# Optimization experiments

Measured on AMD Instinct MI355X. Metric: run time of the kernel, lower is better.

Reference implementation:

```python
import jax, jax.numpy as jnp
import numpy as np

B, N, C, H = 8, 1024, 1024, 16
HD = C // H
SCALE = HD ** -0.5

def setup_inputs() -> dict:
    key = jax.random.key(0)
    k1, k2, k3, k4 = jax.random.split(key, 4)
    x = jax.random.normal(k1, (B, N, C), dtype=jnp.float32)
    # torch nn.Linear weights: [out, in]
    w_qkv = jax.random.normal(k2, (3 * C, C), dtype=jnp.float32) * (C ** -0.5)
    w_proj = jax.random.normal(k3, (C, C), dtype=jnp.float32) * (C ** -0.5)
    b_proj = jax.random.normal(k4, (C,), dtype=jnp.float32) * 0.02
    return {"x": x, "w_qkv": w_qkv, "w_proj": w_proj, "b_proj": b_proj}

def reference(x, w_qkv, w_proj, b_proj):
    Bv, Nv, Cv = x.shape
    # qkv projection (no bias); torch Linear: x @ W^T
    qkv = jnp.einsum('bnc,dc->bnd', x, w_qkv)
    qkv = qkv.reshape(Bv, Nv, 3, H, HD).transpose(2, 0, 3, 1, 4)  # [3,B,H,N,hd]
    q, k, v = qkv[0], qkv[1], qkv[2]
    attn = jnp.einsum('bhnd,bhmd->bhnm', q, k) * SCALE  # [B,H,N,N]
    attn = jax.nn.softmax(attn, axis=-1)
    out = jnp.einsum('bhnm,bhmd->bhnd', attn, v)
    out = out.transpose(0, 2, 1, 3).reshape(Bv, Nv, Cv)
    out = jnp.einsum('bnc,dc->bnd', out, w_proj) + b_proj
    return out
```

## Files before the change

kernel.cpp:

```cpp
#include <hip/hip_runtime.h>


typedef __attribute__((ext_vector_type(8))) short bf16x8;
typedef __attribute__((ext_vector_type(4))) short bf16x4;
typedef __attribute__((ext_vector_type(4))) float f32x4;

__device__ __forceinline__ short f2bf(float f) {
    union { float f; unsigned u; } x;
    x.f = f;
    unsigned r = x.u + 0x7fffu + ((x.u >> 16) & 1u);
    return (short)(r >> 16);
}

__device__ __forceinline__ void load_lds16(const void* g, void* l) {
    __builtin_amdgcn_global_load_lds((const __attribute__((address_space(1))) unsigned*)g,
                                     (__attribute__((address_space(3))) unsigned*)l,
                                     16, 0, 0);
}

__global__ __launch_bounds__(256) void convert_all(const float* __restrict__ x,
                                                   const float* __restrict__ wqkv,
                                                   const float* __restrict__ wproj,
                                                   short* __restrict__ xb,
                                                   short* __restrict__ wqkvb,
                                                   short* __restrict__ wprojb) {
    int i = blockIdx.x * 256 + threadIdx.x;
    const float* src;
    short* dst;
    int j;
    if (i < 2097152)      { src = x;     dst = xb;     j = i; }
    else if (i < 2883584) { src = wqkv;  dst = wqkvb;  j = i - 2097152; }
    else                  { src = wproj; dst = wprojb; j = i - 2883584; }
    float4 v = *(const float4*)(src + j * 4);
    unsigned lo = (unsigned short)f2bf(v.x) | ((unsigned)(unsigned short)f2bf(v.y) << 16);
    unsigned hi = (unsigned short)f2bf(v.z) | ((unsigned)(unsigned short)f2bf(v.w) << 16);
    uint2 p; p.x = lo; p.y = hi;
    *(uint2*)(dst + j * 4) = p;
}

__global__ __launch_bounds__(256) void gemm_qkv(const short* __restrict__ A,
                                                const short* __restrict__ Bt,
                                                short* __restrict__ q,
                                                short* __restrict__ k,
                                                short* __restrict__ vt) {
    __shared__ alignas(16) short As[3][128][32];
    __shared__ alignas(16) short Bs[3][128][32];
    const int K = 1024;
    const int m0 = blockIdx.y * 128;
    const int n0 = blockIdx.x * 128;
    const int t = threadIdx.x;
    const int w = t >> 6, lane = t & 63, quad = lane >> 4, l16 = lane & 15;
    const int wm = (w >> 1) * 64, wn = (w & 1) * 64;
    const int srow = lane >> 2;
    const int sc8 = (lane & 3) * 8;

    const short* Abase = &A[(m0 + w * 32 + srow) * K + sc8];
    const short* Bbase = &Bt[(n0 + w * 32 + srow) * K + sc8];

    f32x4 acc[4][4];
    for (int mi = 0; mi < 4; ++mi)
        for (int ni = 0; ni < 4; ++ni)
            acc[mi][ni] = (f32x4){0.f, 0.f, 0.f, 0.f};

    #pragma unroll
    for (int p = 0; p < 2; ++p) {
        load_lds16(Abase + p * 32,          &As[p][w * 32][0]);
        load_lds16(Abase + 16 * K + p * 32, &As[p][w * 32 + 16][0]);
        load_lds16(Bbase + p * 32,          &Bs[p][w * 32][0]);
        load_lds16(Bbase + 16 * K + p * 32, &Bs[p][w * 32 + 16][0]);
    }

    #pragma unroll
    for (int it = 0; it < 32; ++it) {
        if (it == 31) asm volatile("s_waitcnt vmcnt(0) lgkmcnt(0)" ::: "memory");
        else          asm volatile("s_waitcnt vmcnt(4) lgkmcnt(0)" ::: "memory");
        asm volatile("s_barrier" ::: "memory");
        if (it < 30) {
            const int b2 = (it + 2) % 3;
            load_lds16(Abase + (it + 2) * 32,          &As[b2][w * 32][0]);
            load_lds16(Abase + 16 * K + (it + 2) * 32, &As[b2][w * 32 + 16][0]);
            load_lds16(Bbase + (it + 2) * 32,          &Bs[b2][w * 32][0]);
            load_lds16(Bbase + 16 * K + (it + 2) * 32, &Bs[b2][w * 32 + 16][0]);
        }
        const int cb = it % 3;
        bf16x8 af[4], bfr[4];
        for (int i = 0; i < 4; ++i) af[i]  = *(const bf16x8*)&As[cb][wm + i * 16 + l16][quad * 8];
        for (int i = 0; i < 4; ++i) bfr[i] = *(const bf16x8*)&Bs[cb][wn + i * 16 + l16][quad * 8];
        for (int mi = 0; mi < 4; ++mi)
            for (int ni = 0; ni < 4; ++ni)
                acc[mi][ni] = __builtin_amdgcn_mfma_f32_16x16x32_bf16(af[mi], bfr[ni], acc[mi][ni], 0, 0, 0);
    }

    const float QS = 0.125f * 1.44269504088896f;
    for (int ni = 0; ni < 4; ++ni) {
        int col = n0 + wn + ni * 16 + l16;
        int sect = col >> 10;
        int c = col & 1023;
        int h = c >> 6, d = c & 63;
        for (int mi = 0; mi < 4; ++mi) {
            for (int r = 0; r < 4; ++r) {
                int m = m0 + wm + mi * 16 + quad * 4 + r;
                int b = m >> 10, i = m & 1023;
                float v = acc[mi][ni][r];
                if (sect == 0)      q[((b * 16 + h) * 1024 + i) * 64 + d] = f2bf(v * QS);
                else if (sect == 1) k[((b * 16 + h) * 1024 + i) * 64 + d] = f2bf(v);
                else                vt[((b * 16 + h) * 64 + d) * 1024 + i] = f2bf(v);
            }
        }
    }
}

__global__ __launch_bounds__(256) void attn_kernel(const short* __restrict__ q,
                                                   const short* __restrict__ k,
                                                   const short* __restrict__ vt,
                                                   short* __restrict__ ao) {
    __shared__ alignas(16) short Ks[64][72];
    __shared__ alignas(16) short Vs[64][72];

    const int bh = blockIdx.y, qt = blockIdx.x;
    const int t = threadIdx.x, w = t >> 6, lane = t & 63, quad = lane >> 4, l16 = lane & 15;
    const short* qg = q  + (bh * 1024 + qt * 128) * 64;
    const short* kg = k  + bh * 65536;
    const short* vg = vt + bh * 65536;

    bf16x8 qf[2][2];
    for (int mi = 0; mi < 2; ++mi) {
        const short* qr = qg + (w * 32 + mi * 16 + l16) * 64;
        qf[mi][0] = *(const bf16x8*)(qr + quad * 8);
        qf[mi][1] = *(const bf16x8*)(qr + 32 + quad * 8);
    }

    const int r0 = t >> 3,          c80 = (t & 7) * 8;
    const int r1 = (t + 256) >> 3,  c81 = c80;

    float rs[2] = {0.f, 0.f};
    f32x4 oaccT[2][4];
    for (int mi = 0; mi < 2; ++mi)
        for (int dt = 0; dt < 4; ++dt) oaccT[mi][dt] = (f32x4){0.f, 0.f, 0.f, 0.f};

    {
        float4 a = *(const float4*)&kg[r0 * 64 + c80];
        float4 b = *(const float4*)&kg[r1 * 64 + c81];
        float4 c = *(const float4*)&vg[r0 * 1024 + c80];
        float4 d = *(const float4*)&vg[r1 * 1024 + c81];
        *(float4*)&Ks[r0][c80] = a;  *(float4*)&Ks[r1][c81] = b;
        *(float4*)&Vs[r0][c80] = c;  *(float4*)&Vs[r1][c81] = d;
    }

    for (int jt = 0; jt < 16; ++jt) {
        asm volatile("s_waitcnt lgkmcnt(0)" ::: "memory");
        asm volatile("s_barrier" ::: "memory");

        float4 kr0, kr1, vr0, vr1;
        if (jt < 15) {
            int jn = jt + 1;
            kr0 = *(const float4*)&kg[(jn * 64 + r0) * 64 + c80];
            kr1 = *(const float4*)&kg[(jn * 64 + r1) * 64 + c81];
            vr0 = *(const float4*)&vg[r0 * 1024 + jn * 64 + c80];
            vr1 = *(const float4*)&vg[r1 * 1024 + jn * 64 + c81];
        }

        bf16x8 kf[4][2];
        bf16x4 vtf[4][4];
        for (int js = 0; js < 4; ++js) {
            kf[js][0] = *(const bf16x8*)&Ks[js * 16 + l16][quad * 8];
            kf[js][1] = *(const bf16x8*)&Ks[js * 16 + l16][32 + quad * 8];
            for (int dt = 0; dt < 4; ++dt)
                vtf[js][dt] = *(const bf16x4*)&Vs[dt * 16 + l16][js * 16 + quad * 4];
        }
        asm volatile("s_waitcnt lgkmcnt(0)" ::: "memory");
        asm volatile("s_barrier" ::: "memory");
        if (jt < 15) {
            *(float4*)&Ks[r0][c80] = kr0;  *(float4*)&Ks[r1][c81] = kr1;
            *(float4*)&Vs[r0][c80] = vr0;  *(float4*)&Vs[r1][c81] = vr1;
        }

        for (int mi = 0; mi < 2; ++mi) {
            for (int js = 0; js < 4; ++js) {
                f32x4 s = (f32x4){0.f, 0.f, 0.f, 0.f};
                s = __builtin_amdgcn_mfma_f32_16x16x32_bf16(kf[js][0], qf[mi][0], s, 0, 0, 0);
                s = __builtin_amdgcn_mfma_f32_16x16x32_bf16(kf[js][1], qf[mi][1], s, 0, 0, 0);
                bf16x4 pfrag;
                for (int r = 0; r < 4; ++r) {
                    float p = __builtin_amdgcn_exp2f(s[r]);
                    rs[mi] += p;
                    pfrag[r] = f2bf(p);
                }
                for (int dt = 0; dt < 4; ++dt)
                    oaccT[mi][dt] = __builtin_amdgcn_mfma_f32_16x16x16bf16_1k(
                        vtf[js][dt], pfrag, oaccT[mi][dt], 0, 0, 0);
            }
        }
    }

    for (int mi = 0; mi < 2; ++mi) {
        rs[mi] += __shfl_xor(rs[mi], 16, 64);
        rs[mi] += __shfl_xor(rs[mi], 32, 64);
    }

    const int b = bh >> 4, h = bh & 15;
    for (int mi = 0; mi < 2; ++mi) {
        float inv = 1.0f / rs[mi];
        int i = qt * 128 + w * 32 + mi * 16 + l16;
        short* aor = ao + (b * 1024 + i) * 1024 + h * 64;
        for (int dt = 0; dt < 4; ++dt) {
            bf16x4 o4;
            for (int r = 0; r < 4; ++r) o4[r] = f2bf(oaccT[mi][dt][r] * inv);
            *(bf16x4*)(aor + dt * 16 + quad * 4) = o4;
        }
    }
}

__global__ __launch_bounds__(256) void gemm_proj(const short* __restrict__ A,
                                                 const short* __restrict__ Bt,
                                                 const float* __restrict__ bias,
                                                 float* __restrict__ out) {
    __shared__ alignas(16) short As[3][128][32];
    __shared__ alignas(16) short Bs[3][128][32];
    const int K = 1024;
    const int m0 = blockIdx.y * 128;
    const int n0 = blockIdx.x * 128;
    const int t = threadIdx.x;
    const int w = t >> 6, lane = t & 63, quad = lane >> 4, l16 = lane & 15;
    const int wm = (w >> 1) * 64, wn = (w & 1) * 64;
    const int srow = lane >> 2;
    const int sc8 = (lane & 3) * 8;

    const short* Abase = &A[(m0 + w * 32 + srow) * K + sc8];
    const short* Bbase = &Bt[(n0 + w * 32 + srow) * K + sc8];

    f32x4 acc[4][4];
    for (int mi = 0; mi < 4; ++mi)
        for (int ni = 0; ni < 4; ++ni)
            acc[mi][ni] = (f32x4){0.f, 0.f, 0.f, 0.f};

    #pragma unroll
    for (int p = 0; p < 2; ++p) {
        load_lds16(Abase + p * 32,          &As[p][w * 32][0]);
        load_lds16(Abase + 16 * K + p * 32, &As[p][w * 32 + 16][0]);
        load_lds16(Bbase + p * 32,          &Bs[p][w * 32][0]);
        load_lds16(Bbase + 16 * K + p * 32, &Bs[p][w * 32 + 16][0]);
    }

    #pragma unroll
    for (int it = 0; it < 32; ++it) {
        if (it == 31) asm volatile("s_waitcnt vmcnt(0) lgkmcnt(0)" ::: "memory");
        else          asm volatile("s_waitcnt vmcnt(4) lgkmcnt(0)" ::: "memory");
        asm volatile("s_barrier" ::: "memory");
        if (it < 30) {
            const int b2 = (it + 2) % 3;
            load_lds16(Abase + (it + 2) * 32,          &As[b2][w * 32][0]);
            load_lds16(Abase + 16 * K + (it + 2) * 32, &As[b2][w * 32 + 16][0]);
            load_lds16(Bbase + (it + 2) * 32,          &Bs[b2][w * 32][0]);
            load_lds16(Bbase + 16 * K + (it + 2) * 32, &Bs[b2][w * 32 + 16][0]);
        }
        const int cb = it % 3;
        bf16x8 af[4], bfr[4];
        for (int i = 0; i < 4; ++i) af[i]  = *(const bf16x8*)&As[cb][wm + i * 16 + l16][quad * 8];
        for (int i = 0; i < 4; ++i) bfr[i] = *(const bf16x8*)&Bs[cb][wn + i * 16 + l16][quad * 8];
        for (int mi = 0; mi < 4; ++mi)
            for (int ni = 0; ni < 4; ++ni)
                acc[mi][ni] = __builtin_amdgcn_mfma_f32_16x16x32_bf16(af[mi], bfr[ni], acc[mi][ni], 0, 0, 0);
    }

    for (int ni = 0; ni < 4; ++ni) {
        int col = n0 + wn + ni * 16 + l16;
        float bv = bias[col];
        for (int mi = 0; mi < 4; ++mi) {
            for (int r = 0; r < 4; ++r) {
                int m = m0 + wm + mi * 16 + quad * 4 + r;
                out[m * 1024 + col] = acc[mi][ni][r] + bv;
            }
        }
    }
}

extern "C" void kernel_launch(void* const* d_in, const int* in_sizes, int n_in,
                              void* d_out, int out_size, void* d_ws, size_t ws_size,
                              hipStream_t stream) {
    const float* x      = (const float*)d_in[0];
    const float* w_qkv  = (const float*)d_in[1];
    const float* w_proj = (const float*)d_in[2];
    const float* b_proj = (const float*)d_in[3];
    float* out = (float*)d_out;

    char* ws = (char*)d_ws;
    short* xb     = (short*)(ws);
    short* wqkvb  = (short*)(ws + 16777216);
    short* wprojb = (short*)(ws + 23068672);
    short* qb     = (short*)(ws + 25165824);
    short* kb     = (short*)(ws + 41943040);
    short* vtb    = (short*)(ws + 58720256);
    short* aob    = (short*)(ws + 75497472);

    convert_all<<<12288, 256, 0, stream>>>(x, w_qkv, w_proj, xb, wqkvb, wprojb);
    gemm_qkv<<<dim3(24, 64), 256, 0, stream>>>(xb, wqkvb, qb, kb, vtb);
    attn_kernel<<<dim3(8, 128), 256, 0, stream>>>(qb, kb, vtb, aob);
    gemm_proj<<<dim3(8, 64), 256, 0, stream>>>(aob, wprojb, b_proj, out);
}
```

Before: 267.0 us.

## Double-buffer K/V tiles in LDS to drop the mid-iteration barrier

The attention kernel's K and V shared-memory tiles become two buffers that alternate each iteration. This removes the second barrier per KV tile, and the next tile is written after compute rather than between fragment reads and MFMAs. Fragments are now read per js inside the compute loop, which lowers register pressure but interleaves LDS reads with MFMAs. LDS use doubles, which may affect occupancy.

```diff
diff --git a/kernel.cpp b/kernel.cpp
--- a/kernel.cpp
+++ b/kernel.cpp
@@ -114,8 +114,8 @@
                                                    const short* __restrict__ k,
                                                    const short* __restrict__ vt,
                                                    short* __restrict__ ao) {
-    __shared__ alignas(16) short Ks[64][72];
-    __shared__ alignas(16) short Vs[64][72];
+    __shared__ alignas(16) short Ks[2][64][72];
+    __shared__ alignas(16) short Vs[2][64][72];
 
     const int bh = blockIdx.y, qt = blockIdx.x;
     const int t = threadIdx.x, w = t >> 6, lane = t & 63, quad = lane >> 4, l16 = lane & 15;
@@ -143,11 +143,12 @@
         float4 b = *(const float4*)&kg[r1 * 64 + c81];
         float4 c = *(const float4*)&vg[r0 * 1024 + c80];
         float4 d = *(const float4*)&vg[r1 * 1024 + c81];
-        *(float4*)&Ks[r0][c80] = a;  *(float4*)&Ks[r1][c81] = b;
-        *(float4*)&Vs[r0][c80] = c;  *(float4*)&Vs[r1][c81] = d;
+        *(float4*)&Ks[0][r0][c80] = a;  *(float4*)&Ks[0][r1][c81] = b;
+        *(float4*)&Vs[0][r0][c80] = c;  *(float4*)&Vs[0][r1][c81] = d;
     }
 
     for (int jt = 0; jt < 16; ++jt) {
+        const int cur = jt & 1;
         asm volatile("s_waitcnt lgkmcnt(0)" ::: "memory");
         asm volatile("s_barrier" ::: "memory");
 
@@ -160,26 +161,16 @@
             vr1 = *(const float4*)&vg[r1 * 1024 + jn * 64 + c81];
         }
 
-        bf16x8 kf[4][2];
-        bf16x4 vtf[4][4];
         for (int js = 0; js < 4; ++js) {
-            kf[js][0] = *(const bf16x8*)&Ks[js * 16 + l16][quad * 8];
-            kf[js][1] = *(const bf16x8*)&Ks[js * 16 + l16][32 + quad * 8];
+            bf16x8 kf0 = *(const bf16x8*)&Ks[cur][js * 16 + l16][quad * 8];
+            bf16x8 kf1 = *(const bf16x8*)&Ks[cur][js * 16 + l16][32 + quad * 8];
+            bf16x4 vtf[4];
             for (int dt = 0; dt < 4; ++dt)
-                vtf[js][dt] = *(const bf16x4*)&Vs[dt * 16 + l16][js * 16 + quad * 4];
-        }
-        asm volatile("s_waitcnt lgkmcnt(0)" ::: "memory");
-        asm volatile("s_barrier" ::: "memory");
-        if (jt < 15) {
-            *(float4*)&Ks[r0][c80] = kr0;  *(float4*)&Ks[r1][c81] = kr1;
-            *(float4*)&Vs[r0][c80] = vr0;  *(float4*)&Vs[r1][c81] = vr1;
-        }
-
-        for (int mi = 0; mi < 2; ++mi) {
-            for (int js = 0; js < 4; ++js) {
+                vtf[dt] = *(const bf16x4*)&Vs[cur][dt * 16 + l16][js * 16 + quad * 4];
+            for (int mi = 0; mi < 2; ++mi) {
                 f32x4 s = (f32x4){0.f, 0.f, 0.f, 0.f};
-                s = __builtin_amdgcn_mfma_f32_16x16x32_bf16(kf[js][0], qf[mi][0], s, 0, 0, 0);
-                s = __builtin_amdgcn_mfma_f32_16x16x32_bf16(kf[js][1], qf[mi][1], s, 0, 0, 0);
+                s = __builtin_amdgcn_mfma_f32_16x16x32_bf16(kf0, qf[mi][0], s, 0, 0, 0);
+                s = __builtin_amdgcn_mfma_f32_16x16x32_bf16(kf1, qf[mi][1], s, 0, 0, 0);
                 bf16x4 pfrag;
                 for (int r = 0; r < 4; ++r) {
                     float p = __builtin_amdgcn_exp2f(s[r]);
@@ -188,8 +179,14 @@
                 }
                 for (int dt = 0; dt < 4; ++dt)
                     oaccT[mi][dt] = __builtin_amdgcn_mfma_f32_16x16x16bf16_1k(
-                        vtf[js][dt], pfrag, oaccT[mi][dt], 0, 0, 0);
+                        vtf[dt], pfrag, oaccT[mi][dt], 0, 0, 0);
             }
+        }
+
+        if (jt < 15) {
+            const int nxt = cur ^ 1;
+            *(float4*)&Ks[nxt][r0][c80] = kr0;  *(float4*)&Ks[nxt][r1][c81] = kr1;
+            *(float4*)&Vs[nxt][r0][c80] = vr0;  *(float4*)&Vs[nxt][r1][c81] = vr1;
         }
     }
 
```

After: 265.6 us. No clear change (-0.5%).
